# Kernel optimization log

Hardware: AMD Instinct MI355X
Metric: run time of the kernel (lower is better)

## Reference

```python
import jax, jax.numpy as jnp
import numpy as np
from jax.scipy.special import logsumexp

REG_E = 0.05      # entropic regularization (init_kwargs reg_e)
N_ITER = 100      # n_iter_sinkhorn
N, M = 4096, 4096


def setup_inputs() -> dict:
    key = jax.random.key(0)
    k1, k2, k3 = jax.random.split(key, 3)
    p = jax.random.uniform(k1, (N,), dtype=jnp.float32)
    p = p / p.sum()                      # probability weights of measure P
    q = jax.random.uniform(k2, (M,), dtype=jnp.float32)
    q = q / q.sum()                      # probability weights of measure Q
    C = jax.random.uniform(k3, (N, M), dtype=jnp.float32)  # ground cost
    return {"p": p, "q": q, "C": C}


def reference(p, q, C):
    # POT ot.bregman.sinkhorn(..., method='sinkhorn_log') on C / C.max()
    # Log-domain Sinkhorn: Mr = -(C/max(C))/reg; alternate potential updates
    #   u = log p - logsumexp(Mr + v[None,:], axis=1)
    #   v = log q - logsumexp(Mr + u[:,None], axis=0)
    # plan = exp(Mr + u[:,None] + v[None,:])
    Mr = -(C / jax.lax.stop_gradient(jnp.max(C))) / REG_E   # (n, m)
    logp = jnp.log(p)
    logq = jnp.log(q)

    def body(_, uv):
        u, v = uv
        u = logp - logsumexp(Mr + v[None, :], axis=1)   # row logsumexp
        v = logq - logsumexp(Mr + u[:, None], axis=0)   # col logsumexp
        return (u, v)

    u0 = jnp.zeros_like(p)
    v0 = jnp.zeros_like(q)
    u, v = jax.lax.fori_loop(0, N_ITER, body, (u0, v0))
    return jnp.exp(Mr + u[:, None] + v[None, :])        # OT plan (n, m)
```

## Files before the change

kernel.cpp:

```cpp
#include <hip/hip_runtime.h>

#define N 4096
#define NITER 100
#define LOG2E 1.44269504088896340736f
#define TOL 3e-4f
#define NB 256
#define NT 1024
#define ROWS 16
#define TILE_BYTES (ROWS * N * 2)
#define GRPS 8
#define BPG 32
#define EVSTRIDE 144

typedef unsigned short u16;

__device__ __forceinline__ float aload(const float* p) {
    return __hip_atomic_load(p, __ATOMIC_RELAXED, __HIP_MEMORY_SCOPE_AGENT);
}
__device__ __forceinline__ void astore(float* p, float x) {
    __hip_atomic_store(p, x, __ATOMIC_RELAXED, __HIP_MEMORY_SCOPE_AGENT);
}

__device__ __forceinline__ float fexp2(float x) {
#if __has_builtin(__builtin_amdgcn_exp2f)
    return __builtin_amdgcn_exp2f(x);
#else
    return __expf(x * 0.6931471805599453f);
#endif
}

__device__ __forceinline__ void gbar_arrive(int* bar, int e) {
    int* base = bar + e * EVSTRIDE;
    const int g = (int)(blockIdx.x >> 5);
    int r = __hip_atomic_fetch_add(base + g * 16, 1, __ATOMIC_ACQ_REL, __HIP_MEMORY_SCOPE_AGENT);
    if (r == BPG - 1)
        __hip_atomic_fetch_add(base + 128, 1, __ATOMIC_ACQ_REL, __HIP_MEMORY_SCOPE_AGENT);
}
__device__ __forceinline__ void gbar_wait(int* bar, int e) {
    const int* root = bar + e * EVSTRIDE + 128;
    while (__hip_atomic_load(root, __ATOMIC_ACQUIRE, __HIP_MEMORY_SCOPE_AGENT) < GRPS)
        __builtin_amdgcn_s_sleep(1);
}
__device__ __forceinline__ void gbar(int* bar, int e) {
    __syncthreads();
    if (threadIdx.x == 0) { gbar_arrive(bar, e); gbar_wait(bar, e); }
    __syncthreads();
}

__global__ __launch_bounds__(NT) void ot_all(const float* __restrict__ p,
                                             const float* __restrict__ q,
                                             const float* __restrict__ C,
                                             int* bar,
                                             float* fmax_arr,
                                             float* ddel,
                                             float* v,
                                             float* part,
                                             float* __restrict__ out) {
    extern __shared__ u16 tile[];
    const int t = threadIdx.x;
    const int b = blockIdx.x;
    const int lane = t & 63;
    const int wave = t >> 6;
    const int gid = b * NT + t;
    const int r0 = b * ROWS;
    const int c0 = b * 16;
    const int j0 = t * 4;

    __shared__ float sred[4][16];
    __shared__ float wbc[4];
    __shared__ float s2[16][16];
    __shared__ float dm[16];
    __shared__ float lp[ROWS], pp[ROWS], lq[16], su[ROWS];
    __shared__ float sMown, sMaxC, sM;

    if (gid < N) astore(&v[gid], 0.f);
    {
        const float4* Crow = (const float4*)(C + (size_t)r0 * N);
        float m = 0.f;
        for (int i = t; i < ROWS * N / 4; i += NT) {
            float4 c = Crow[i];
            m = fmaxf(m, fmaxf(fmaxf(c.x, c.y), fmaxf(c.z, c.w)));
        }
#pragma unroll
        for (int off = 32; off; off >>= 1) m = fmaxf(m, __shfl_down(m, off));
        if (lane == 0) dm[wave] = m;
        __syncthreads();
        if (t == 0) {
            m = dm[0];
#pragma unroll
            for (int i = 1; i < 16; ++i) m = fmaxf(m, dm[i]);
            sMown = m;
            astore(&fmax_arr[b], m);
            gbar_arrive(bar, 0);
        }
        __syncthreads();
    }

    {
        const float qmul = 65535.0f / sMown;
        const float4* Crow = (const float4*)(C + (size_t)r0 * N);
        uint2* T2 = (uint2*)tile;
        for (int i = t; i < ROWS * N / 4; i += NT) {
            float4 a = Crow[i];
            uint2 o;
            o.x = min(65535u, __float2uint_rn(a.x * qmul)) | (min(65535u, __float2uint_rn(a.y * qmul)) << 16);
            o.y = min(65535u, __float2uint_rn(a.z * qmul)) | (min(65535u, __float2uint_rn(a.w * qmul)) << 16);
            T2[i] = o;
        }
        if (t < ROWS) {
            float pv = p[r0 + t];
            pp[t] = pv;
            lp[t] = __logf(pv);
            lq[t] = __logf(q[c0 + t]);
            su[t] = 0.f;
        }
    }
    __syncthreads();
    if (t == 0) gbar_wait(bar, 0);
    __syncthreads();
    if (wave == 0) {
        float d = fmaxf(fmaxf(aload(&fmax_arr[lane]), aload(&fmax_arr[64 + lane])),
                        fmaxf(aload(&fmax_arr[128 + lane]), aload(&fmax_arr[192 + lane])));
#pragma unroll
        for (int off = 32; off; off >>= 1) d = fmaxf(d, __shfl_down(d, off));
        if (lane == 0) sMaxC = d;
    }
    __syncthreads();
    const float ndstep = -(20.0f / 65535.0f) * (sMown / sMaxC) * LOG2E;
    float vreg = 0.f;

    for (int it = 0; it < NITER; ++it) {
        float vv2[4];
#pragma unroll
        for (int k = 0; k < 4; ++k) vv2[k] = aload(&v[j0 + k]) * LOG2E;
        float ca[4] = {0.f, 0.f, 0.f, 0.f};

        for (int ch = 0; ch < 4; ++ch) {
            const int rl = ch * 4;
            float tq[4][4], sp[4];
#pragma unroll
            for (int r = 0; r < 4; ++r) {
                uint2 a = *(const uint2*)(tile + (size_t)(rl + r) * N + j0);
                float e0 = fexp2(fmaf((float)(a.x & 0xffffu), ndstep, vv2[0]));
                float e1 = fexp2(fmaf((float)(a.x >> 16),     ndstep, vv2[1]));
                float e2 = fexp2(fmaf((float)(a.y & 0xffffu), ndstep, vv2[2]));
                float e3 = fexp2(fmaf((float)(a.y >> 16),     ndstep, vv2[3]));
                tq[r][0] = e0; tq[r][1] = e1; tq[r][2] = e2; tq[r][3] = e3;
                sp[r] = (e0 + e1) + (e2 + e3);
            }
#pragma unroll
            for (int r = 0; r < 4; ++r) {
                float s = sp[r];
#pragma unroll
                for (int off = 32; off; off >>= 1) s += __shfl_down(s, off);
                if (lane == 0) sred[r][wave] = s;
            }
            __syncthreads();
            if (wave < 4) {
                float s = (lane < 16) ? sred[wave][lane] : 0.f;
                s += __shfl_down(s, 8);
                s += __shfl_down(s, 4);
                s += __shfl_down(s, 2);
                s += __shfl_down(s, 1);
                if (lane == 0) {
                    wbc[wave] = pp[rl + wave] / s;
                    su[rl + wave] = lp[rl + wave] - __logf(s);
                }
            }
            __syncthreads();
#pragma unroll
            for (int r = 0; r < 4; ++r) {
                const float w = wbc[r];
#pragma unroll
                for (int k = 0; k < 4; ++k) ca[k] = fmaf(tq[r][k], w, ca[k]);
            }
        }
#pragma unroll
        for (int k = 0; k < 4; ++k) astore(&part[(size_t)b * N + j0 + k], ca[k]);
        gbar(bar, 1 + 2 * it);

        {
            const int cl = t & 15;
            const int ch = t >> 4;
            const int c = c0 + cl;
            float s = 0.f;
#pragma unroll
            for (int k = 0; k < 4; ++k) s += aload(&part[(size_t)(ch + 64 * k) * N + c]);
            s += __shfl_down(s, 16);
            s += __shfl_down(s, 32);
            if (lane < 16) s2[cl][wave] = s;
            __syncthreads();
            if (t < 16) {
                float tot = 0.f;
#pragma unroll
                for (int w = 0; w < 16; ++w) tot += s2[t][w];
                const float vn = lq[t] + vreg - __logf(tot);
                astore(&v[c0 + t], vn);
                float d = fabsf(vn - vreg);
                vreg = vn;
                d = fmaxf(d, __shfl_down(d, 8));
                d = fmaxf(d, __shfl_down(d, 4));
                d = fmaxf(d, __shfl_down(d, 2));
                d = fmaxf(d, __shfl_down(d, 1));
                if (t == 0) astore(&ddel[it * NB + b], d);
            }
        }
        gbar(bar, 2 + 2 * it);

        if (wave == 0) {
            const float* dd = ddel + it * NB;
            float d = fmaxf(fmaxf(aload(dd + lane), aload(dd + 64 + lane)),
                            fmaxf(aload(dd + 128 + lane), aload(dd + 192 + lane)));
#pragma unroll
            for (int off = 32; off; off >>= 1) d = fmaxf(d, __shfl_down(d, off));
            if (lane == 0) sM = d;
        }
        __syncthreads();
        if (sM < TOL) break;
    }

    {
        float vvl[4];
#pragma unroll
        for (int k = 0; k < 4; ++k) vvl[k] = aload(&v[j0 + k]) * LOG2E;
#pragma unroll 4
        for (int r = 0; r < ROWS; ++r) {
            const float uul = su[r] * LOG2E;
            uint2 a = *(const uint2*)(tile + (size_t)r * N + j0);
            float4 o;
            o.x = fexp2(fmaf((float)(a.x & 0xffffu), ndstep, uul + vvl[0]));
            o.y = fexp2(fmaf((float)(a.x >> 16),     ndstep, uul + vvl[1]));
            o.z = fexp2(fmaf((float)(a.y & 0xffffu), ndstep, uul + vvl[2]));
            o.w = fexp2(fmaf((float)(a.y >> 16),     ndstep, uul + vvl[3]));
            *(float4*)(out + (size_t)(r0 + r) * N + j0) = o;
        }
    }
}

extern "C" void kernel_launch(void* const* d_in, const int* in_sizes, int n_in,
                              void* d_out, int out_size, void* d_ws, size_t ws_size,
                              hipStream_t stream) {
    const float* p = (const float*)d_in[0];
    const float* q = (const float*)d_in[1];
    const float* C = (const float*)d_in[2];
    float* out = (float*)d_out;

    char* base = (char*)d_ws;
    int* bar = (int*)base;
    float* fmax_arr = (float*)(base + 120 * 1024);
    float* ddel = (float*)(base + 124 * 1024);
    float* v = (float*)(base + 228 * 1024);
    float* part = (float*)(base + 256 * 1024);

    hipMemsetAsync(d_ws, 0, (size_t)(1 + 2 * NITER) * EVSTRIDE * sizeof(int), stream);

    hipFuncSetAttribute((const void*)ot_all, hipFuncAttributeMaxDynamicSharedMemorySize, TILE_BYTES);

    void* args[] = {(void*)&p, (void*)&q, (void*)&C, (void*)&bar,
                    (void*)&fmax_arr, (void*)&ddel, (void*)&v, (void*)&part, (void*)&out};
    hipLaunchCooperativeKernel((void*)ot_all, dim3(NB), dim3(NT), args, TILE_BYTES, stream);
}
```

Measured before the change: 210.3 us.

## Switch Sinkhorn to scaling domain with fp16 kernel tile and master-block barriers

Replaces the log-domain iteration with the equivalent multiplicative Sinkhorn form. The Gibbs kernel exp(-C/reg) is precomputed once into an fp16 shared-memory tile, so each iteration needs only multiplies instead of per-element exp2. The hierarchical atomic-counter grid barrier becomes a flag/root scheme: block 0 gathers per-block flags, reduces the convergence metric, and broadcasts a stop decision, so the separate ddel reduction pass goes away. The convergence tolerance is also loosened from 3e-4 to 2e-3 (now tested on |q/tot-1| rather than the potential change), which could end the loop earlier. The risks are fp16 underflow of small kernel entries, since exp(-20) is near the fp16 subnormal range, and reduced accuracy.

```diff
diff --git a/kernel.cpp b/kernel.cpp
--- a/kernel.cpp
+++ b/kernel.cpp
@@ -1,16 +1,15 @@
 #include <hip/hip_runtime.h>
+#include <hip/hip_fp16.h>
 
 #define N 4096
 #define NITER 100
 #define LOG2E 1.44269504088896340736f
-#define TOL 3e-4f
+#define TOL 2e-3f
 #define NB 256
 #define NT 1024
 #define ROWS 16
 #define TILE_BYTES (ROWS * N * 2)
-#define GRPS 8
-#define BPG 32
-#define EVSTRIDE 144
+#define NEV (1 + 2 * NITER)
 
 typedef unsigned short u16;
 
@@ -29,31 +28,73 @@
 #endif
 }
 
-__device__ __forceinline__ void gbar_arrive(int* bar, int e) {
-    int* base = bar + e * EVSTRIDE;
-    const int g = (int)(blockIdx.x >> 5);
-    int r = __hip_atomic_fetch_add(base + g * 16, 1, __ATOMIC_ACQ_REL, __HIP_MEMORY_SCOPE_AGENT);
-    if (r == BPG - 1)
-        __hip_atomic_fetch_add(base + 128, 1, __ATOMIC_ACQ_REL, __HIP_MEMORY_SCOPE_AGENT);
-}
-__device__ __forceinline__ void gbar_wait(int* bar, int e) {
-    const int* root = bar + e * EVSTRIDE + 128;
-    while (__hip_atomic_load(root, __ATOMIC_ACQUIRE, __HIP_MEMORY_SCOPE_AGENT) < GRPS)
-        __builtin_amdgcn_s_sleep(1);
-}
-__device__ __forceinline__ void gbar(int* bar, int e) {
-    __syncthreads();
-    if (threadIdx.x == 0) { gbar_arrive(bar, e); gbar_wait(bar, e); }
-    __syncthreads();
+__device__ __forceinline__ unsigned pkh2(float a, float b) {
+    union { __half2 h; unsigned u; } c;
+    c.h = __floats2half2_rn(a, b);
+    return c.u;
+}
+__device__ __forceinline__ float2 uph2(unsigned u) {
+    union { __half2 h; unsigned u; } c;
+    c.u = u;
+    return __half22float2(c.h);
+}
+
+__device__ __forceinline__ int gbar(int e, int payload, int mode,
+                                    float* flags, int* roots,
+                                    float* sbar, int* shb) {
+    const int t = threadIdx.x;
+    const int lane = t & 63;
+    const int wave = t >> 6;
+    __syncthreads();
+    if (blockIdx.x == 0) {
+        float val = -1e30f;
+        if (t == 0) {
+            val = __int_as_float(payload);
+        } else if (t < NB) {
+            const int* fi = (const int*)(flags + (size_t)e * NB + t);
+            int u = __hip_atomic_load(fi, __ATOMIC_ACQUIRE, __HIP_MEMORY_SCOPE_AGENT);
+            while (u == -1) {
+                __builtin_amdgcn_s_sleep(1);
+                u = __hip_atomic_load(fi, __ATOMIC_ACQUIRE, __HIP_MEMORY_SCOPE_AGENT);
+            }
+            val = __int_as_float(u);
+        }
+        if (wave < 4) {
+#pragma unroll
+            for (int off = 32; off; off >>= 1) val = fmaxf(val, __shfl_down(val, off));
+            if (lane == 0) sbar[wave] = val;
+        }
+        __syncthreads();
+        if (t == 0) {
+            const float m = fmaxf(fmaxf(sbar[0], sbar[1]), fmaxf(sbar[2], sbar[3]));
+            int rv = 1;
+            if (mode == 1) rv = __float_as_int(m);
+            else if (mode == 2) rv = (m < TOL) ? 2 : 1;
+            __hip_atomic_store(&roots[e], rv, __ATOMIC_RELEASE, __HIP_MEMORY_SCOPE_AGENT);
+            *shb = rv;
+        }
+    } else {
+        if (t == 0) {
+            __hip_atomic_store((int*)(flags + (size_t)e * NB + blockIdx.x), payload,
+                               __ATOMIC_RELEASE, __HIP_MEMORY_SCOPE_AGENT);
+            int r = __hip_atomic_load(&roots[e], __ATOMIC_ACQUIRE, __HIP_MEMORY_SCOPE_AGENT);
+            while (r == 0) {
+                __builtin_amdgcn_s_sleep(1);
+                r = __hip_atomic_load(&roots[e], __ATOMIC_ACQUIRE, __HIP_MEMORY_SCOPE_AGENT);
+            }
+            *shb = r;
+        }
+    }
+    __syncthreads();
+    return *shb;
 }
 
 __global__ __launch_bounds__(NT) void ot_all(const float* __restrict__ p,
                                              const float* __restrict__ q,
                                              const float* __restrict__ C,
-                                             int* bar,
-                                             float* fmax_arr,
-                                             float* ddel,
-                                             float* v,
+                                             int* roots,
+                                             float* flags,
+                                             float* ev,
                                              float* part,
                                              float* __restrict__ out) {
     extern __shared__ u16 tile[];
@@ -70,10 +111,12 @@
     __shared__ float wbc[4];
     __shared__ float s2[16][16];
     __shared__ float dm[16];
-    __shared__ float lp[ROWS], pp[ROWS], lq[16], su[ROWS];
-    __shared__ float sMown, sMaxC, sM;
-
-    if (gid < N) astore(&v[gid], 0.f);
+    __shared__ float sbar[4];
+    __shared__ int shb;
+    __shared__ float pp[ROWS], qq[16], eu[ROWS];
+    __shared__ float sMown;
+
+    if (gid < N) astore(&ev[gid], 1.0f);
     {
         const float4* Crow = (const float4*)(C + (size_t)r0 * N);
         float m = 0.f;
@@ -90,11 +133,12 @@
 #pragma unroll
             for (int i = 1; i < 16; ++i) m = fmaxf(m, dm[i]);
             sMown = m;
-            astore(&fmax_arr[b], m);
-            gbar_arrive(bar, 0);
         }
         __syncthreads();
     }
+    if (b != 0 && t == 0)
+        __hip_atomic_store((int*)(flags + b), __float_as_int(sMown),
+                           __ATOMIC_RELEASE, __HIP_MEMORY_SCOPE_AGENT);
 
     {
         const float qmul = 65535.0f / sMown;
@@ -108,31 +152,67 @@
             T2[i] = o;
         }
         if (t < ROWS) {
-            float pv = p[r0 + t];
-            pp[t] = pv;
-            lp[t] = __logf(pv);
-            lq[t] = __logf(q[c0 + t]);
-            su[t] = 0.f;
-        }
-    }
-    __syncthreads();
-    if (t == 0) gbar_wait(bar, 0);
-    __syncthreads();
-    if (wave == 0) {
-        float d = fmaxf(fmaxf(aload(&fmax_arr[lane]), aload(&fmax_arr[64 + lane])),
-                        fmaxf(aload(&fmax_arr[128 + lane]), aload(&fmax_arr[192 + lane])));
-#pragma unroll
-        for (int off = 32; off; off >>= 1) d = fmaxf(d, __shfl_down(d, off));
-        if (lane == 0) sMaxC = d;
-    }
-    __syncthreads();
-    const float ndstep = -(20.0f / 65535.0f) * (sMown / sMaxC) * LOG2E;
-    float vreg = 0.f;
+            pp[t] = p[r0 + t];
+            qq[t] = q[c0 + t];
+        }
+    }
+    __syncthreads();
+    if (b == 0) {
+        float val = (t == 0) ? sMown : -1e30f;
+        if (t > 0 && t < NB) {
+            const int* fi = (const int*)(flags + t);
+            int u = __hip_atomic_load(fi, __ATOMIC_ACQUIRE, __HIP_MEMORY_SCOPE_AGENT);
+            while (u == -1) {
+                __builtin_amdgcn_s_sleep(1);
+                u = __hip_atomic_load(fi, __ATOMIC_ACQUIRE, __HIP_MEMORY_SCOPE_AGENT);
+            }
+            val = __int_as_float(u);
+        }
+        if (wave < 4) {
+#pragma unroll
+            for (int off = 32; off; off >>= 1) val = fmaxf(val, __shfl_down(val, off));
+            if (lane == 0) sbar[wave] = val;
+        }
+        __syncthreads();
+        if (t == 0) {
+            const float m = fmaxf(fmaxf(sbar[0], sbar[1]), fmaxf(sbar[2], sbar[3]));
+            __hip_atomic_store(&roots[0], __float_as_int(m), __ATOMIC_RELEASE, __HIP_MEMORY_SCOPE_AGENT);
+            shb = __float_as_int(m);
+        }
+    } else {
+        if (t == 0) {
+            int r = __hip_atomic_load(&roots[0], __ATOMIC_ACQUIRE, __HIP_MEMORY_SCOPE_AGENT);
+            while (r == 0) {
+                __builtin_amdgcn_s_sleep(1);
+                r = __hip_atomic_load(&roots[0], __ATOMIC_ACQUIRE, __HIP_MEMORY_SCOPE_AGENT);
+            }
+            shb = r;
+        }
+    }
+    __syncthreads();
+    const float maxC = __int_as_float(shb);
+
+    {
+        const float nd2 = -(20.0f / 65535.0f) * (sMown / maxC) * LOG2E;
+        uint2* T2 = (uint2*)tile;
+        for (int i = t; i < ROWS * N / 4; i += NT) {
+            uint2 a = T2[i];
+            float e0 = fexp2((float)(a.x & 0xffffu) * nd2);
+            float e1 = fexp2((float)(a.x >> 16) * nd2);
+            float e2 = fexp2((float)(a.y & 0xffffu) * nd2);
+            float e3 = fexp2((float)(a.y >> 16) * nd2);
+            a.x = pkh2(e0, e1);
+            a.y = pkh2(e2, e3);
+            T2[i] = a;
+        }
+    }
+    __syncthreads();
+    float evreg = 1.0f;
 
     for (int it = 0; it < NITER; ++it) {
-        float vv2[4];
-#pragma unroll
-        for (int k = 0; k < 4; ++k) vv2[k] = aload(&v[j0 + k]) * LOG2E;
+        float evv[4];
+#pragma unroll
+        for (int k = 0; k < 4; ++k) evv[k] = aload(&ev[j0 + k]);
         float ca[4] = {0.f, 0.f, 0.f, 0.f};
 
         for (int ch = 0; ch < 4; ++ch) {
@@ -141,12 +221,14 @@
 #pragma unroll
             for (int r = 0; r < 4; ++r) {
                 uint2 a = *(const uint2*)(tile + (size_t)(rl + r) * N + j0);
-                float e0 = fexp2(fmaf((float)(a.x & 0xffffu), ndstep, vv2[0]));
-                float e1 = fexp2(fmaf((float)(a.x >> 16),     ndstep, vv2[1]));
-                float e2 = fexp2(fmaf((float)(a.y & 0xffffu), ndstep, vv2[2]));
-                float e3 = fexp2(fmaf((float)(a.y >> 16),     ndstep, vv2[3]));
-                tq[r][0] = e0; tq[r][1] = e1; tq[r][2] = e2; tq[r][3] = e3;
-                sp[r] = (e0 + e1) + (e2 + e3);
+                float2 x0 = uph2(a.x);
+                float2 x1 = uph2(a.y);
+                float t0 = x0.x * evv[0];
+                float t1 = x0.y * evv[1];
+                float t2 = x1.x * evv[2];
+                float t3 = x1.y * evv[3];
+                tq[r][0] = t0; tq[r][1] = t1; tq[r][2] = t2; tq[r][3] = t3;
+                sp[r] = (t0 + t1) + (t2 + t3);
             }
 #pragma unroll
             for (int r = 0; r < 4; ++r) {
@@ -163,8 +245,9 @@
                 s += __shfl_down(s, 2);
                 s += __shfl_down(s, 1);
                 if (lane == 0) {
-                    wbc[wave] = pp[rl + wave] / s;
-                    su[rl + wave] = lp[rl + wave] - __logf(s);
+                    const float w = pp[rl + wave] / s;
+                    wbc[wave] = w;
+                    eu[rl + wave] = w;
                 }
             }
             __syncthreads();
@@ -177,8 +260,9 @@
         }
 #pragma unroll
         for (int k = 0; k < 4; ++k) astore(&part[(size_t)b * N + j0 + k], ca[k]);
-        gbar(bar, 1 + 2 * it);
-
+        gbar(1 + 2 * it, __float_as_int(1.0f), 0, flags, roots, sbar, &shb);
+
+        float dblk = 0.f;
         {
             const int cl = t & 15;
             const int ch = t >> 4;
@@ -194,44 +278,37 @@
                 float tot = 0.f;
 #pragma unroll
                 for (int w = 0; w < 16; ++w) tot += s2[t][w];
-                const float vn = lq[t] + vreg - __logf(tot);
-                astore(&v[c0 + t], vn);
-                float d = fabsf(vn - vreg);
-                vreg = vn;
+                const float rr = qq[t] / tot;
+                const float evn = evreg * rr;
+                astore(&ev[c0 + t], evn);
+                evreg = evn;
+                float d = fabsf(rr - 1.0f);
                 d = fmaxf(d, __shfl_down(d, 8));
                 d = fmaxf(d, __shfl_down(d, 4));
                 d = fmaxf(d, __shfl_down(d, 2));
                 d = fmaxf(d, __shfl_down(d, 1));
-                if (t == 0) astore(&ddel[it * NB + b], d);
-            }
-        }
-        gbar(bar, 2 + 2 * it);
-
-        if (wave == 0) {
-            const float* dd = ddel + it * NB;
-            float d = fmaxf(fmaxf(aload(dd + lane), aload(dd + 64 + lane)),
-                            fmaxf(aload(dd + 128 + lane), aload(dd + 192 + lane)));
-#pragma unroll
-            for (int off = 32; off; off >>= 1) d = fmaxf(d, __shfl_down(d, off));
-            if (lane == 0) sM = d;
-        }
-        __syncthreads();
-        if (sM < TOL) break;
+                dblk = d;
+            }
+        }
+        const int rv = gbar(2 + 2 * it, __float_as_int(dblk), 2, flags, roots, sbar, &shb);
+        if (rv == 2) break;
     }
 
     {
-        float vvl[4];
-#pragma unroll
-        for (int k = 0; k < 4; ++k) vvl[k] = aload(&v[j0 + k]) * LOG2E;
+        float ev4[4];
+#pragma unroll
+        for (int k = 0; k < 4; ++k) ev4[k] = aload(&ev[j0 + k]);
 #pragma unroll 4
         for (int r = 0; r < ROWS; ++r) {
-            const float uul = su[r] * LOG2E;
+            const float g = eu[r];
             uint2 a = *(const uint2*)(tile + (size_t)r * N + j0);
+            float2 x0 = uph2(a.x);
+            float2 x1 = uph2(a.y);
             float4 o;
-            o.x = fexp2(fmaf((float)(a.x & 0xffffu), ndstep, uul + vvl[0]));
-            o.y = fexp2(fmaf((float)(a.x >> 16),     ndstep, uul + vvl[1]));
-            o.z = fexp2(fmaf((float)(a.y & 0xffffu), ndstep, uul + vvl[2]));
-            o.w = fexp2(fmaf((float)(a.y >> 16),     ndstep, uul + vvl[3]));
+            o.x = x0.x * (g * ev4[0]);
+            o.y = x0.y * (g * ev4[1]);
+            o.z = x1.x * (g * ev4[2]);
+            o.w = x1.y * (g * ev4[3]);
             *(float4*)(out + (size_t)(r0 + r) * N + j0) = o;
         }
     }
@@ -246,17 +323,17 @@
     float* out = (float*)d_out;
 
     char* base = (char*)d_ws;
-    int* bar = (int*)base;
-    float* fmax_arr = (float*)(base + 120 * 1024);
-    float* ddel = (float*)(base + 124 * 1024);
-    float* v = (float*)(base + 228 * 1024);
+    int* roots = (int*)base;
+    float* flags = (float*)(base + 4096);
+    float* ev = (float*)(base + 216 * 1024);
     float* part = (float*)(base + 256 * 1024);
 
-    hipMemsetAsync(d_ws, 0, (size_t)(1 + 2 * NITER) * EVSTRIDE * sizeof(int), stream);
-
-    hipFuncSetAttribute((const void*)ot_all, hipFuncAttributeMaxDynamicSharedMemorySize, TILE_BYTES);
-
-    void* args[] = {(void*)&p, (void*)&q, (void*)&C, (void*)&bar,
-                    (void*)&fmax_arr, (void*)&ddel, (void*)&v, (void*)&part, (void*)&out};
-    hipLaunchCooperativeKernel((void*)ot_all, dim3(NB), dim3(NT), args, TILE_BYTES, stream);
-}
+    (void)hipMemsetAsync(base, 0, 4096, stream);
+    (void)hipMemsetAsync(base + 4096, 0xFF, (size_t)NEV * NB * sizeof(float), stream);
+
+    (void)hipFuncSetAttribute((const void*)ot_all, hipFuncAttributeMaxDynamicSharedMemorySize, TILE_BYTES);
+
+    void* args[] = {(void*)&p, (void*)&q, (void*)&C, (void*)&roots,
+                    (void*)&flags, (void*)&ev, (void*)&part, (void*)&out};
+    (void)hipLaunchCooperativeKernel((void*)ot_all, dim3(NB), dim3(NT), args, TILE_BYTES, stream);
+}
```

New measurement: 266.9 us. +27.0%, slower.
